# Optimization experiments

Hardware: AMD Instinct MI355X
Metric: run time of the kernel (lower is better)

The kernel has to match this reference:

```python
import jax, jax.numpy as jnp
import numpy as np

UNITS = 1024
D = 1024

def setup_inputs() -> dict:
    key = jax.random.key(0)
    ks = jax.random.split(key, 8)
    B, T = 32, 2048
    query = jax.random.normal(ks[0], (B, D), dtype=jnp.float32)
    values = jax.random.normal(ks[1], (B, T, D), dtype=jnp.float32)
    s1 = 1.0 / np.sqrt(D)
    s2 = 1.0 / np.sqrt(UNITS)
    W1 = jax.random.normal(ks[2], (D, UNITS), dtype=jnp.float32) * s1
    b1 = jnp.zeros((UNITS,), dtype=jnp.float32)
    W2 = jax.random.normal(ks[3], (D, UNITS), dtype=jnp.float32) * s1
    b2 = jnp.zeros((UNITS,), dtype=jnp.float32)
    Wv = jax.random.normal(ks[4], (UNITS, 1), dtype=jnp.float32) * s2
    bv = jnp.zeros((1,), dtype=jnp.float32)
    return {"query": query, "values": values, "W1": W1, "b1": b1,
            "W2": W2, "b2": b2, "Wv": Wv, "bv": bv}

def reference(query, values, W1, b1, W2, b2, Wv, bv):
    # query: [B, D]; values: [B, T, D]
    q_proj = query @ W1 + b1                     # [B, U]
    v_proj = jnp.einsum('btd,du->btu', values, W2) + b2  # [B, T, U]
    h = jnp.tanh(q_proj[:, None, :] + v_proj)    # [B, T, U]
    score = jnp.einsum('btu,uo->bto', h, Wv) + bv  # [B, T, 1]
    attention_weights = jax.nn.softmax(score, axis=1)  # [B, T, 1]
    context_vector = jnp.sum(attention_weights * values, axis=1)  # [B, D]
    return (context_vector, attention_weights)
```

## Files before the change

kernel.cpp:

```cpp
#include <hip/hip_runtime.h>
#include <hip/hip_bf16.h>
#include <stdint.h>


typedef unsigned short ushort_t;
typedef short bf16x8 __attribute__((ext_vector_type(8)));
typedef float f32x4 __attribute__((ext_vector_type(4)));

#define GLOBAL_AS __attribute__((address_space(1)))
#define LDS_AS    __attribute__((address_space(3)))

__device__ __forceinline__ ushort_t f2bf(float f) {
    union { float f; unsigned int u; } v;
    v.f = f;
    unsigned int u = v.u;
    unsigned int r = u + 0x7FFFu + ((u >> 16) & 1u);
    return (ushort_t)(r >> 16);
}
__device__ __forceinline__ unsigned int pk2(float a, float b) {
    union { __hip_bfloat162 h; unsigned int u; } c;
    c.h = __float22bfloat162_rn(make_float2(a, b));
    return c.u;
}
__device__ __forceinline__ float fast_tanh(float x) {
    float ax = __builtin_fabsf(x);
    float e = __expf(-2.0f * ax);
    float t = (1.0f - e) * __builtin_amdgcn_rcpf(1.0f + e);
    return __builtin_copysignf(t, x);
}

static constexpr int B_ = 32, T_ = 2048, D_ = 1024, U_ = 1024;
static constexpr int M_ = B_ * T_;
static constexpr int TRANS_B = 1024;
static constexpr int QPROJ_B = 64;

__global__ __launch_bounds__(256) void k_prep(const float* __restrict__ W2,
                                              const float* __restrict__ query,
                                              const float* __restrict__ W1,
                                              const float* __restrict__ b1,
                                              const float* __restrict__ b2,
                                              ushort_t* __restrict__ W2T,
                                              float* __restrict__ qpb) {
    __shared__ float smem[8192 + 4 * 64 * 9];
    int bid = blockIdx.x;
    const int tid = threadIdx.x;

    if (bid < TRANS_B) {
        float(*tile)[33] = (float(*)[33])smem;
        int u0 = (bid & 31) * 32, d0 = (bid >> 5) * 32;
        int tx = tid & 31, ty = tid >> 5;
#pragma unroll
        for (int r = 0; r < 4; ++r)
            tile[ty + r * 8][tx] = W2[(size_t)(d0 + ty + r * 8) * U_ + (u0 + tx)];
        __syncthreads();
#pragma unroll
        for (int r = 0; r < 4; ++r)
            W2T[(size_t)(u0 + ty + r * 8) * D_ + (d0 + tx)] = f2bf(tile[tx][ty + r * 8]);
        return;
    }
    const int qb = bid - TRANS_B;
    const int bg = qb >> 4;
    const int uc = qb & 15;

    float* qs = smem;
    float(*red)[64][9] = (float(*)[64][9])(smem + 8192);

    for (int i = tid; i < 8 * 1024; i += 256)
        qs[i] = query[(size_t)(bg * 8 + (i >> 10)) * D_ + (i & 1023)];
    __syncthreads();

    const int ul = tid & 63, ds = tid >> 6;
    const int u = uc * 64 + ul;
    float acc[8] = {0.f, 0.f, 0.f, 0.f, 0.f, 0.f, 0.f, 0.f};
#pragma unroll 8
    for (int d = ds * 256; d < ds * 256 + 256; ++d) {
        const float w = W1[(size_t)d * U_ + u];
#pragma unroll
        for (int b = 0; b < 8; ++b) acc[b] += qs[(b << 10) + d] * w;
    }
#pragma unroll
    for (int b = 0; b < 8; ++b) red[ds][ul][b] = acc[b];
    __syncthreads();
    for (int i = tid; i < 512; i += 256) {
        const int b = i & 7, uu = i >> 3;
        const float s = (red[0][uu][b] + red[1][uu][b]) + (red[2][uu][b] + red[3][uu][b]);
        const int ug = uc * 64 + uu;
        qpb[(size_t)(bg * 8 + b) * U_ + ug] = s + b1[ug] + b2[ug];
    }
}

#define BM 128
#define BN 128
#define BK 64

__global__ __launch_bounds__(256) void k_score_gemm(const float* __restrict__ values,
                                                    const ushort_t* __restrict__ W2T,
                                                    const float* __restrict__ qpb,
                                                    const float* __restrict__ Wv,
                                                    float* __restrict__ scores_partial) {
    __shared__ ushort_t As[BM * BK];
    __shared__ ushort_t Bs[BN * BK];
    __shared__ float sScore[BM];

    const int tid = threadIdx.x;
    const int lane = tid & 63;
    const int w = tid >> 6;
    const int wm = w >> 1, wn = w & 1;

    const int g = blockIdx.x;
    const int mt = ((g >> 6) << 3) | (g & 7);
    const int nt = (g >> 3) & 7;
    const int m0 = mt * BM, n0 = nt * BN;

    if (tid < BM) sScore[tid] = 0.f;

    f32x4 acc[4][4];
#pragma unroll
    for (int i = 0; i < 4; ++i)
#pragma unroll
        for (int j = 0; j < 4; ++j) acc[i][j] = (f32x4){0.f, 0.f, 0.f, 0.f};

    const int lr = lane >> 3;
    const int cB = (lane & 7) ^ lr;
    const ushort_t* bBase = W2T + (size_t)(n0 + w * 8 + lr) * D_ + cB * 8;

    const int rA = tid >> 3;
    const int cA = tid & 7;
    const int pA = cA ^ (rA & 7);
    const float* aSrc = values + (size_t)(m0 + rA) * D_ + cA * 8;
    ushort_t* aDst = As + rA * BK + pA * 8;

    const int quad = lane >> 4;
    const int l15 = lane & 15;
    const int l7 = l15 & 7;

    f32x4 ra0[4], ra1[4];
#pragma unroll
    for (int i = 0; i < 4; ++i) {
        ra0[i] = *(const f32x4*)(aSrc + (size_t)i * 32 * D_);
        ra1[i] = *(const f32x4*)(aSrc + (size_t)i * 32 * D_ + 4);
    }

    for (int k0 = 0; k0 < D_; k0 += BK) {
#pragma unroll
        for (int i = 0; i < 4; ++i) {
            __builtin_amdgcn_global_load_lds(
                (const GLOBAL_AS void*)(bBase + k0 + (size_t)i * 32 * D_),
                (LDS_AS void*)(Bs + i * 2048 + w * 512), 16, 0, 0);
        }
#pragma unroll
        for (int i = 0; i < 4; ++i) {
            uint4 p;
            p.x = pk2(ra0[i][0], ra0[i][1]);
            p.y = pk2(ra0[i][2], ra0[i][3]);
            p.z = pk2(ra1[i][0], ra1[i][1]);
            p.w = pk2(ra1[i][2], ra1[i][3]);
            *(uint4*)(aDst + i * 32 * BK) = p;
        }
        __syncthreads();
        if (k0 + BK < D_) {
#pragma unroll
            for (int i = 0; i < 4; ++i) {
                ra0[i] = *(const f32x4*)(aSrc + k0 + BK + (size_t)i * 32 * D_);
                ra1[i] = *(const f32x4*)(aSrc + k0 + BK + (size_t)i * 32 * D_ + 4);
            }
        }
#pragma unroll
        for (int kk = 0; kk < BK; kk += 32) {
            bf16x8 af[4], bfr[4];
            const int cb = kk >> 3;
#pragma unroll
            for (int i = 0; i < 4; ++i) {
                int r = wm * 64 + i * 16 + l15;
                af[i] = *(const bf16x8*)(As + (r << 6) + (((quad + cb) ^ l7) << 3));
            }
#pragma unroll
            for (int j = 0; j < 4; ++j) {
                int r = wn * 64 + j * 16 + l15;
                bfr[j] = *(const bf16x8*)(Bs + (r << 6) + (((quad + cb) ^ l7) << 3));
            }
#pragma unroll
            for (int i = 0; i < 4; ++i)
#pragma unroll
                for (int j = 0; j < 4; ++j)
                    acc[i][j] = __builtin_amdgcn_mfma_f32_16x16x32_bf16(
                        af[i], bfr[j], acc[i][j], 0, 0, 0);
        }
        __syncthreads();
    }

    const int b = m0 >> 11;
    const float* qp = qpb + b * U_;
    float qv[4], wv[4];
#pragma unroll
    for (int j = 0; j < 4; ++j) {
        int u = n0 + wn * 64 + j * 16 + l15;
        qv[j] = qp[u];
        wv[j] = Wv[u];
    }
#pragma unroll
    for (int i = 0; i < 4; ++i) {
#pragma unroll
        for (int r = 0; r < 4; ++r) {
            float s = 0.f;
#pragma unroll
            for (int j = 0; j < 4; ++j) s += fast_tanh(acc[i][j][r] + qv[j]) * wv[j];
            s += __shfl_xor(s, 1);
            s += __shfl_xor(s, 2);
            s += __shfl_xor(s, 4);
            s += __shfl_xor(s, 8);
            if (l15 == 0) atomicAdd(&sScore[wm * 64 + i * 16 + quad * 4 + r], s);
        }
    }
    __syncthreads();
    if (tid < BM) scores_partial[(size_t)(m0 + tid) * 8 + nt] = sScore[tid];
}

__global__ __launch_bounds__(256) void k_softmax(const float* __restrict__ scores_partial,
                                                 const float* __restrict__ bv,
                                                 float* __restrict__ w_f,
                                                 float* __restrict__ out_w) {
    const int b = blockIdx.x;
    __shared__ float s[T_];
    __shared__ float red[4];
    const int tid = threadIdx.x;
    const float bvf = bv[0];

    float lmax = -1e30f;
    for (int t = tid; t < T_; t += 256) {
        const float* p = scores_partial + (size_t)(b * T_ + t) * 8;
        float sc = ((p[0] + p[1]) + (p[2] + p[3])) + ((p[4] + p[5]) + (p[6] + p[7])) + bvf;
        s[t] = sc;
        lmax = fmaxf(lmax, sc);
    }
    for (int off = 32; off; off >>= 1) lmax = fmaxf(lmax, __shfl_xor(lmax, off));
    if ((tid & 63) == 0) red[tid >> 6] = lmax;
    __syncthreads();
    const float gmax = fmaxf(fmaxf(red[0], red[1]), fmaxf(red[2], red[3]));

    float lsum = 0.f;
    for (int t = tid; t < T_; t += 256) {
        float e = __expf(s[t] - gmax);
        s[t] = e;
        lsum += e;
    }
    for (int off = 32; off; off >>= 1) lsum += __shfl_xor(lsum, off);
    __syncthreads();
    if ((tid & 63) == 0) red[tid >> 6] = lsum;
    __syncthreads();
    const float ginv = 1.f / ((red[0] + red[1]) + (red[2] + red[3]));

    for (int t = tid; t < T_; t += 256) {
        float wgt = s[t] * ginv;
        w_f[b * T_ + t] = wgt;
        out_w[b * T_ + t] = wgt;
    }
}

__global__ __launch_bounds__(256) void k_ctx(const float* __restrict__ values,
                                             const float* __restrict__ w_f,
                                             float* __restrict__ ctx_part) {
    const int tc = blockIdx.x;
    const int b = blockIdx.y;
    const int tid = threadIdx.x;
    __shared__ float wls[128];
    if (tid < 128) wls[tid] = w_f[b * T_ + tc * 128 + tid];
    __syncthreads();

    f32x4 acc = (f32x4){0.f, 0.f, 0.f, 0.f};
    const float* base = values + (size_t)(b * T_ + tc * 128) * D_ + tid * 4;
#pragma unroll 4
    for (int tt = 0; tt < 128; ++tt)
        acc += wls[tt] * *(const f32x4*)(base + (size_t)tt * D_);
    *(f32x4*)(ctx_part + ((size_t)(tc * 32 + b) << 10) + tid * 4) = acc;
}

__global__ __launch_bounds__(256) void k_ctx_fin(const float* __restrict__ ctx_part,
                                                 float* __restrict__ out_ctx) {
    const int b = blockIdx.x;
    const int tid = threadIdx.x;
    f32x4 s = (f32x4){0.f, 0.f, 0.f, 0.f};
#pragma unroll
    for (int tc = 0; tc < 16; ++tc)
        s += *(const f32x4*)(ctx_part + ((size_t)(tc * 32 + b) << 10) + tid * 4);
    *(f32x4*)(out_ctx + b * D_ + tid * 4) = s;
}

extern "C" void kernel_launch(void* const* d_in, const int* in_sizes, int n_in,
                              void* d_out, int out_size, void* d_ws, size_t ws_size,
                              hipStream_t stream) {
    const float* query  = (const float*)d_in[0];
    const float* values = (const float*)d_in[1];
    const float* W1     = (const float*)d_in[2];
    const float* b1     = (const float*)d_in[3];
    const float* W2     = (const float*)d_in[4];
    const float* b2     = (const float*)d_in[5];
    const float* Wv     = (const float*)d_in[6];
    const float* bv     = (const float*)d_in[7];

    float* out_ctx = (float*)d_out;
    float* out_w   = out_ctx + B_ * D_;

    char* ws = (char*)d_ws;
    const size_t OFF_W2T = 0;
    const size_t OFF_QPB = 0x200000;
    const size_t OFF_SP  = 0x220000;
    const size_t OFF_WF  = 0x420000;
    const size_t OFF_CP  = 0x460000;

    ushort_t* W2T            = (ushort_t*)(ws + OFF_W2T);
    float*    qpb            = (float*)(ws + OFF_QPB);
    float*    scores_partial = (float*)(ws + OFF_SP);
    float*    w_f            = (float*)(ws + OFF_WF);
    float*    ctx_part       = (float*)(ws + OFF_CP);

    k_prep<<<dim3(TRANS_B + QPROJ_B), 256, 0, stream>>>(W2, query, W1, b1, b2, W2T, qpb);
    k_score_gemm<<<dim3((M_ / BM) * (U_ / BN)), 256, 0, stream>>>(
        values, W2T, qpb, Wv, scores_partial);
    k_softmax<<<dim3(B_), 256, 0, stream>>>(scores_partial, bv, w_f, out_w);
    k_ctx<<<dim3(16, B_), 256, 0, stream>>>(values, w_f, ctx_part);
    k_ctx_fin<<<dim3(B_), 256, 0, stream>>>(ctx_part, out_ctx);

    (void)in_sizes; (void)n_in; (void)out_size; (void)ws_size;
}
```

Before: 607.2 us.

## Pre-convert values to bf16 and fuse softmax, context and final reduction

A prep pass now converts the whole values tensor to bf16 in the workspace, so the score GEMM can stream A tiles straight into LDS with async global-to-LDS loads instead of loading fp32 into registers and packing them in the loop. The softmax, context and final-sum kernels are merged into one grid of 16×32 blocks. Each block recomputes the per-batch softmax and handles one T chunk, and the last block per batch, found with an atomic counter, does the final reduction. The cost is an extra full read of fp32 values plus a write of a 128MB bf16 copy, and redundant softmax work in each block.

```diff
diff --git a/kernel.cpp b/kernel.cpp
--- a/kernel.cpp
+++ b/kernel.cpp
@@ -33,19 +33,24 @@
 static constexpr int M_ = B_ * T_;
 static constexpr int TRANS_B = 1024;
 static constexpr int QPROJ_B = 64;
+static constexpr int CONV_B  = 4096;
 
 __global__ __launch_bounds__(256) void k_prep(const float* __restrict__ W2,
                                               const float* __restrict__ query,
                                               const float* __restrict__ W1,
                                               const float* __restrict__ b1,
                                               const float* __restrict__ b2,
+                                              const float* __restrict__ values,
                                               ushort_t* __restrict__ W2T,
-                                              float* __restrict__ qpb) {
+                                              float* __restrict__ qpb,
+                                              ushort_t* __restrict__ vb,
+                                              unsigned int* __restrict__ cnt) {
     __shared__ float smem[8192 + 4 * 64 * 9];
     int bid = blockIdx.x;
     const int tid = threadIdx.x;
 
     if (bid < TRANS_B) {
+        if (bid == 0 && tid < B_) cnt[tid] = 0u;
         float(*tile)[33] = (float(*)[33])smem;
         int u0 = (bid & 31) * 32, d0 = (bid >> 5) * 32;
         int tx = tid & 31, ty = tid >> 5;
@@ -58,9 +63,29 @@
             W2T[(size_t)(u0 + ty + r * 8) * D_ + (d0 + tx)] = f2bf(tile[tx][ty + r * 8]);
         return;
     }
-    const int qb = bid - TRANS_B;
-    const int bg = qb >> 4;
-    const int uc = qb & 15;
+    bid -= TRANS_B;
+
+    if (bid >= QPROJ_B) {
+        const int cb = bid - QPROJ_B;
+        const size_t base = (size_t)cb * 2048 + tid;
+#pragma unroll
+        for (int k = 0; k < 8; ++k) {
+            const size_t chunk = base + (size_t)k * 256;
+            const float* s = values + chunk * 8;
+            f32x4 v0 = *(const f32x4*)s;
+            f32x4 v1 = *(const f32x4*)(s + 4);
+            uint4 p;
+            p.x = pk2(v0[0], v0[1]);
+            p.y = pk2(v0[2], v0[3]);
+            p.z = pk2(v1[0], v1[1]);
+            p.w = pk2(v1[2], v1[3]);
+            *(uint4*)(vb + chunk * 8) = p;
+        }
+        return;
+    }
+
+    const int bg = bid >> 4;
+    const int uc = bid & 15;
 
     float* qs = smem;
     float(*red)[64][9] = (float(*)[64][9])(smem + 8192);
@@ -93,7 +118,7 @@
 #define BN 128
 #define BK 64
 
-__global__ __launch_bounds__(256) void k_score_gemm(const float* __restrict__ values,
+__global__ __launch_bounds__(256) void k_score_gemm(const ushort_t* __restrict__ vb,
                                                     const ushort_t* __restrict__ W2T,
                                                     const float* __restrict__ qpb,
                                                     const float* __restrict__ Wv,
@@ -121,25 +146,13 @@
         for (int j = 0; j < 4; ++j) acc[i][j] = (f32x4){0.f, 0.f, 0.f, 0.f};
 
     const int lr = lane >> 3;
-    const int cB = (lane & 7) ^ lr;
-    const ushort_t* bBase = W2T + (size_t)(n0 + w * 8 + lr) * D_ + cB * 8;
-
-    const int rA = tid >> 3;
-    const int cA = tid & 7;
-    const int pA = cA ^ (rA & 7);
-    const float* aSrc = values + (size_t)(m0 + rA) * D_ + cA * 8;
-    ushort_t* aDst = As + rA * BK + pA * 8;
+    const int cS = (lane & 7) ^ lr;
+    const ushort_t* bBase = W2T + (size_t)(n0 + w * 8 + lr) * D_ + cS * 8;
+    const ushort_t* aBase = vb + (size_t)(m0 + w * 8 + lr) * D_ + cS * 8;
 
     const int quad = lane >> 4;
     const int l15 = lane & 15;
     const int l7 = l15 & 7;
-
-    f32x4 ra0[4], ra1[4];
-#pragma unroll
-    for (int i = 0; i < 4; ++i) {
-        ra0[i] = *(const f32x4*)(aSrc + (size_t)i * 32 * D_);
-        ra1[i] = *(const f32x4*)(aSrc + (size_t)i * 32 * D_ + 4);
-    }
 
     for (int k0 = 0; k0 < D_; k0 += BK) {
 #pragma unroll
@@ -150,21 +163,11 @@
         }
 #pragma unroll
         for (int i = 0; i < 4; ++i) {
-            uint4 p;
-            p.x = pk2(ra0[i][0], ra0[i][1]);
-            p.y = pk2(ra0[i][2], ra0[i][3]);
-            p.z = pk2(ra1[i][0], ra1[i][1]);
-            p.w = pk2(ra1[i][2], ra1[i][3]);
-            *(uint4*)(aDst + i * 32 * BK) = p;
+            __builtin_amdgcn_global_load_lds(
+                (const GLOBAL_AS void*)(aBase + k0 + (size_t)i * 32 * D_),
+                (LDS_AS void*)(As + i * 2048 + w * 512), 16, 0, 0);
         }
         __syncthreads();
-        if (k0 + BK < D_) {
-#pragma unroll
-            for (int i = 0; i < 4; ++i) {
-                ra0[i] = *(const f32x4*)(aSrc + k0 + BK + (size_t)i * 32 * D_);
-                ra1[i] = *(const f32x4*)(aSrc + k0 + BK + (size_t)i * 32 * D_ + 4);
-            }
-        }
 #pragma unroll
         for (int kk = 0; kk < BK; kk += 32) {
             bf16x8 af[4], bfr[4];
@@ -216,14 +219,20 @@
     if (tid < BM) scores_partial[(size_t)(m0 + tid) * 8 + nt] = sScore[tid];
 }
 
-__global__ __launch_bounds__(256) void k_softmax(const float* __restrict__ scores_partial,
-                                                 const float* __restrict__ bv,
-                                                 float* __restrict__ w_f,
-                                                 float* __restrict__ out_w) {
-    const int b = blockIdx.x;
+__global__ __launch_bounds__(256) void k_smax_ctx(const float* __restrict__ scores_partial,
+                                                  const float* __restrict__ bv,
+                                                  const float* __restrict__ values,
+                                                  float* __restrict__ ctx_part,
+                                                  unsigned int* __restrict__ cnt,
+                                                  float* __restrict__ out_w,
+                                                  float* __restrict__ out_ctx) {
+    const int tc = blockIdx.x;
+    const int b = blockIdx.y;
+    const int tid = threadIdx.x;
     __shared__ float s[T_];
     __shared__ float red[4];
-    const int tid = threadIdx.x;
+    __shared__ float wls[128];
+    __shared__ unsigned int is_last;
     const float bvf = bv[0];
 
     float lmax = -1e30f;
@@ -250,21 +259,11 @@
     __syncthreads();
     const float ginv = 1.f / ((red[0] + red[1]) + (red[2] + red[3]));
 
-    for (int t = tid; t < T_; t += 256) {
-        float wgt = s[t] * ginv;
-        w_f[b * T_ + t] = wgt;
-        out_w[b * T_ + t] = wgt;
-    }
-}
-
-__global__ __launch_bounds__(256) void k_ctx(const float* __restrict__ values,
-                                             const float* __restrict__ w_f,
-                                             float* __restrict__ ctx_part) {
-    const int tc = blockIdx.x;
-    const int b = blockIdx.y;
-    const int tid = threadIdx.x;
-    __shared__ float wls[128];
-    if (tid < 128) wls[tid] = w_f[b * T_ + tc * 128 + tid];
+    if (tid < 128) {
+        float wgt = s[tc * 128 + tid] * ginv;
+        wls[tid] = wgt;
+        out_w[b * T_ + tc * 128 + tid] = wgt;
+    }
     __syncthreads();
 
     f32x4 acc = (f32x4){0.f, 0.f, 0.f, 0.f};
@@ -273,17 +272,19 @@
     for (int tt = 0; tt < 128; ++tt)
         acc += wls[tt] * *(const f32x4*)(base + (size_t)tt * D_);
     *(f32x4*)(ctx_part + ((size_t)(tc * 32 + b) << 10) + tid * 4) = acc;
-}
-
-__global__ __launch_bounds__(256) void k_ctx_fin(const float* __restrict__ ctx_part,
-                                                 float* __restrict__ out_ctx) {
-    const int b = blockIdx.x;
-    const int tid = threadIdx.x;
-    f32x4 s = (f32x4){0.f, 0.f, 0.f, 0.f};
-#pragma unroll
-    for (int tc = 0; tc < 16; ++tc)
-        s += *(const f32x4*)(ctx_part + ((size_t)(tc * 32 + b) << 10) + tid * 4);
-    *(f32x4*)(out_ctx + b * D_ + tid * 4) = s;
+
+    __threadfence();
+    if (tid == 0) is_last = (atomicAdd(&cnt[b], 1u) == 15u) ? 1u : 0u;
+    __syncthreads();
+    if (is_last) {
+        __threadfence();
+        f32x4 ssum = (f32x4){0.f, 0.f, 0.f, 0.f};
+#pragma unroll
+        for (int q = 0; q < 16; ++q)
+            ssum += *(const f32x4*)(ctx_part + ((size_t)(q * 32 + b) << 10) + tid * 4);
+        *(f32x4*)(out_ctx + b * D_ + tid * 4) = ssum;
+        if (tid == 0) cnt[b] = 0u;
+    }
 }
 
 extern "C" void kernel_launch(void* const* d_in, const int* in_sizes, int n_in,
@@ -305,21 +306,22 @@
     const size_t OFF_W2T = 0;
     const size_t OFF_QPB = 0x200000;
     const size_t OFF_SP  = 0x220000;
-    const size_t OFF_WF  = 0x420000;
-    const size_t OFF_CP  = 0x460000;
-
-    ushort_t* W2T            = (ushort_t*)(ws + OFF_W2T);
-    float*    qpb            = (float*)(ws + OFF_QPB);
-    float*    scores_partial = (float*)(ws + OFF_SP);
-    float*    w_f            = (float*)(ws + OFF_WF);
-    float*    ctx_part       = (float*)(ws + OFF_CP);
-
-    k_prep<<<dim3(TRANS_B + QPROJ_B), 256, 0, stream>>>(W2, query, W1, b1, b2, W2T, qpb);
+    const size_t OFF_CNT = 0x420000;
+    const size_t OFF_VB  = 0x500000;
+
+    ushort_t*     W2T            = (ushort_t*)(ws + OFF_W2T);
+    float*        ctx_part       = (float*)(ws + OFF_W2T);
+    float*        qpb            = (float*)(ws + OFF_QPB);
+    float*        scores_partial = (float*)(ws + OFF_SP);
+    unsigned int* cnt            = (unsigned int*)(ws + OFF_CNT);
+    ushort_t*     vb             = (ushort_t*)(ws + OFF_VB);
+
+    k_prep<<<dim3(TRANS_B + QPROJ_B + CONV_B), 256, 0, stream>>>(
+        W2, query, W1, b1, b2, values, W2T, qpb, vb, cnt);
     k_score_gemm<<<dim3((M_ / BM) * (U_ / BN)), 256, 0, stream>>>(
-        values, W2T, qpb, Wv, scores_partial);
-    k_softmax<<<dim3(B_), 256, 0, stream>>>(scores_partial, bv, w_f, out_w);
-    k_ctx<<<dim3(16, B_), 256, 0, stream>>>(values, w_f, ctx_part);
-    k_ctx_fin<<<dim3(B_), 256, 0, stream>>>(ctx_part, out_ctx);
+        vb, W2T, qpb, Wv, scores_partial);
+    k_smax_ctx<<<dim3(16, B_), 256, 0, stream>>>(
+        scores_partial, bv, values, ctx_part, cnt, out_w, out_ctx);
 
     (void)in_sizes; (void)n_in; (void)out_size; (void)ws_size;
 }
```

After: 703.1 us. 1.16x slower.
